# Optimization experiments

Measured on AMD Instinct MI355X. Metric: run time of the kernel, lower is better.

Reference implementation:

```python
import jax, jax.numpy as jnp
import numpy as np

B = 1024
P = 9            # patch_length
D = 2700         # d_model = input_dims = 30*30*3, num_heads=1 so d_k = D
DFF = 512
EPS = 1e-5


def setup_inputs() -> dict:
    key = jax.random.key(0)
    ks = jax.random.split(key, 32)
    s = 0.02
    inp = {
        "state": jax.random.normal(ks[0], (B, P * D), jnp.float32),
        "H1": jax.random.normal(ks[1], (B, P, DFF), jnp.float32),
        "H2": jax.random.normal(ks[2], (B, P, DFF), jnp.float32),
        # main projections: (in, out) layout for x @ W
        "Wq": jax.random.normal(ks[3], (D, D), jnp.float32) * s,
        "bq": jnp.zeros((D,), jnp.float32),
        "Wk": jax.random.normal(ks[4], (D, D), jnp.float32) * s,
        "bk": jnp.zeros((D,), jnp.float32),
        "Wv": jax.random.normal(ks[5], (D, D), jnp.float32) * s,
        "bv": jnp.zeros((D,), jnp.float32),
        # aux modulation projections from dff -> d_model
        "WC1q": jax.random.normal(ks[6], (DFF, D), jnp.float32) * s,
        "bC1q": jnp.zeros((D,), jnp.float32),
        "WC1k": jax.random.normal(ks[7], (DFF, D), jnp.float32) * s,
        "bC1k": jnp.zeros((D,), jnp.float32),
        "WC1v": jax.random.normal(ks[8], (DFF, D), jnp.float32) * s,
        "bC1v": jnp.zeros((D,), jnp.float32),
        "WC2q": jax.random.normal(ks[9], (DFF, D), jnp.float32) * s,
        "bC2q": jnp.zeros((D,), jnp.float32),
        "WC2k": jax.random.normal(ks[10], (DFF, D), jnp.float32) * s,
        "bC2k": jnp.zeros((D,), jnp.float32),
        "WC2v": jax.random.normal(ks[11], (DFF, D), jnp.float32) * s,
        "bC2v": jnp.zeros((D,), jnp.float32),
        # LayerNorm (norm1) affine params
        "gamma": jnp.ones((D,), jnp.float32),
        "beta": jnp.zeros((D,), jnp.float32),
    }
    return inp


def _layernorm(x, gamma, beta):
    mu = jnp.mean(x, axis=-1, keepdims=True)
    var = jnp.mean(jnp.square(x - mu), axis=-1, keepdims=True)
    return (x - mu) * jax.lax.rsqrt(var + EPS) * gamma + beta


def reference(state, H1, H2, Wq, bq, Wk, bk, Wv, bv,
              WC1q, bC1q, WC1k, bC1k, WC1v, bC1v,
              WC2q, bC2q, WC2k, bC2k, WC2v, bC2v,
              gamma, beta):
    x = state.reshape(-1, P, D)  # (B, 9, 2700)
    # elementwise-modulated Q/K/V (num_heads == 1)
    q = (x @ Wq + bq) * ((H1 @ WC1q + bC1q) + (H2 @ WC2q + bC2q))
    k = (x @ Wk + bk) * ((H1 @ WC1k + bC1k) + (H2 @ WC2k + bC2k))
    v = (x @ Wv + bv) * ((H1 @ WC1v + bC1v) + (H2 @ WC2v + bC2v))
    scale = 1.0 / jnp.sqrt(jnp.asarray(D, jnp.float32))
    scores = jnp.einsum("bqd,bkd->bqk", q, k) * scale  # (B, 9, 9)
    A = jax.nn.softmax(scores, axis=-1)
    attn = jnp.einsum("bqk,bkd->bqd", A, v)
    Z1 = x + attn  # dropout is identity in eval
    return _layernorm(Z1, gamma, beta)
```

## Files before the change

### kernel.cpp

```cpp
#include <hip/hip_runtime.h>
#include <stdint.h>


#define MROWS  9216
#define NCOLS  8192
#define KP1    2752
#define KP2    1024
#define DMODEL 2700

typedef __bf16 bf16x8 __attribute__((ext_vector_type(8)));
typedef float  f32x4  __attribute__((ext_vector_type(4)));

__device__ __forceinline__ float b2f(unsigned short u) {
  union { unsigned int u; float f; } v; v.u = ((unsigned int)u) << 16; return v.f;
}
__device__ __forceinline__ unsigned short f2b(float f) {
  union { float f; unsigned int u; } v; v.f = f;
  unsigned int r = v.u + 0x7FFFu + ((v.u >> 16) & 1u);
  return (unsigned short)(r >> 16);
}

__device__ __forceinline__ void gl2lds16(const void* g, void* l) {
  __builtin_amdgcn_global_load_lds(
      (const __attribute__((address_space(1))) void*)g,
      (__attribute__((address_space(3))) void*)l, 16, 0, 0);
}


__global__ void cvt_x(const float* __restrict__ src, unsigned short* __restrict__ dst) {
  int idx = blockIdx.x * 256 + threadIdx.x;
  int r = idx / KP1;
  int c = idx - r * KP1;
  float v = (c < DMODEL) ? src[(size_t)r * DMODEL + c] : 0.f;
  dst[idx] = f2b(v);
}

__global__ void cvt_h(const float* __restrict__ H1, const float* __restrict__ H2,
                      unsigned short* __restrict__ dst) {
  int idx = blockIdx.x * 256 + threadIdx.x;
  int r = idx >> 10, c = idx & 1023;
  float v = (c < 512) ? H1[r * 512 + c] : H2[r * 512 + (c - 512)];
  dst[idx] = f2b(v);
}

__global__ void cvt_wqkv(const float* __restrict__ Wq, const float* __restrict__ Wk,
                         const float* __restrict__ Wv, unsigned short* __restrict__ Wt) {
  __shared__ float tile[32][33];
  int k0 = blockIdx.x * 32, n0 = blockIdx.y * 32;
  int tx = threadIdx.x, ty = threadIdx.y;
#pragma unroll
  for (int s = 0; s < 4; s++) {
    int kk = k0 + ty + 8 * s, nn = n0 + tx;
    float v = 0.f;
    if (kk < DMODEL && nn < 3 * DMODEL) {
      int sec = (nn >= 5400) ? 2 : ((nn >= 2700) ? 1 : 0);
      int d = nn - sec * DMODEL;
      const float* W = (sec == 0) ? Wq : ((sec == 1) ? Wk : Wv);
      v = W[(size_t)kk * DMODEL + d];
    }
    tile[ty + 8 * s][tx] = v;
  }
  __syncthreads();
#pragma unroll
  for (int s = 0; s < 4; s++) {
    int nn = n0 + ty + 8 * s, kk = k0 + tx;
    Wt[(size_t)nn * KP1 + kk] = f2b(tile[tx][ty + 8 * s]);
  }
}

__global__ void cvt_wc(const float* __restrict__ C1q, const float* __restrict__ C1k,
                       const float* __restrict__ C1v, const float* __restrict__ C2q,
                       const float* __restrict__ C2k, const float* __restrict__ C2v,
                       unsigned short* __restrict__ Wt) {
  __shared__ float tile[32][33];
  int k0 = blockIdx.x * 32, n0 = blockIdx.y * 32;
  int tx = threadIdx.x, ty = threadIdx.y;
#pragma unroll
  for (int s = 0; s < 4; s++) {
    int kk = k0 + ty + 8 * s, nn = n0 + tx;
    float v = 0.f;
    if (nn < 3 * DMODEL) {
      int sec = (nn >= 5400) ? 2 : ((nn >= 2700) ? 1 : 0);
      int d = nn - sec * DMODEL;
      const float* W;
      int kr = kk;
      if (kk < 512) {
        W = (sec == 0) ? C1q : ((sec == 1) ? C1k : C1v);
      } else {
        W = (sec == 0) ? C2q : ((sec == 1) ? C2k : C2v);
        kr = kk - 512;
      }
      v = W[(size_t)kr * DMODEL + d];
    }
    tile[ty + 8 * s][tx] = v;
  }
  __syncthreads();
#pragma unroll
  for (int s = 0; s < 4; s++) {
    int nn = n0 + ty + 8 * s, kk = k0 + tx;
    Wt[(size_t)nn * KP2 + kk] = f2b(tile[tx][ty + 8 * s]);
  }
}

__global__ __launch_bounds__(256, 2) void gemm_fused(
    const unsigned short* __restrict__ Xb,
    const unsigned short* __restrict__ Wt,
    const unsigned short* __restrict__ Hb,
    const unsigned short* __restrict__ WCt,
    unsigned short* __restrict__ MQ,
    const float* __restrict__ bq_, const float* __restrict__ bk_, const float* __restrict__ bv_,
    const float* __restrict__ b1q, const float* __restrict__ b1k, const float* __restrict__ b1v,
    const float* __restrict__ b2q, const float* __restrict__ b2k, const float* __restrict__ b2v)
{
  __shared__ __align__(16) unsigned short As[128 * 64];
  __shared__ __align__(16) unsigned short Bs[128 * 64];
  const int tid = threadIdx.x;
  const int wave = tid >> 6, lane = tid & 63;
  const int m0 = blockIdx.y * 128, n0 = blockIdx.x * 128;
  const int wm = (wave >> 1) * 64, wn = (wave & 1) * 64;
  const int lm = lane & 15, lq = lane >> 4, l7 = lane & 7;

  int prow[4], pcl[4];
  unsigned int ldsoff[4];
#pragma unroll
  for (int r = 0; r < 4; r++) {
    int p = r * 256 + tid;
    prow[r] = p >> 3;
    pcl[r] = ((p & 7) ^ (prow[r] & 7)) * 8;
    ldsoff[r] = (unsigned int)p * 8;
  }

  f32x4 acc[4][4];
#pragma unroll
  for (int i = 0; i < 4; i++)
#pragma unroll
    for (int j = 0; j < 4; j++) acc[i][j] = (f32x4){0.f, 0.f, 0.f, 0.f};

  for (int k0 = 0; k0 < KP2; k0 += 64) {
#pragma unroll
    for (int r = 0; r < 4; r++) {
      gl2lds16(Hb + (size_t)(m0 + prow[r]) * KP2 + pcl[r] + k0, As + ldsoff[r]);
      gl2lds16(WCt + (size_t)(n0 + prow[r]) * KP2 + pcl[r] + k0, Bs + ldsoff[r]);
    }
    __syncthreads();
#pragma unroll
    for (int c = 0; c < 2; c++) {
      bf16x8 af[4], bfr[4];
      const int kx = (c * 4 + lq) ^ l7;
#pragma unroll
      for (int t = 0; t < 4; t++) {
        af[t]  = *(const bf16x8*)(As + (((wm + t * 16 + lm) << 3) + kx) * 8);
        bfr[t] = *(const bf16x8*)(Bs + (((wn + t * 16 + lm) << 3) + kx) * 8);
      }
#pragma unroll
      for (int mt = 0; mt < 4; mt++)
#pragma unroll
        for (int nt = 0; nt < 4; nt++)
          acc[mt][nt] = __builtin_amdgcn_mfma_f32_16x16x32_bf16(
              af[mt], bfr[nt], acc[mt][nt], 0, 0, 0);
    }
    __syncthreads();
  }

  unsigned int modp[4][4][2];
#pragma unroll
  for (int nt = 0; nt < 4; nt++) {
    int gc = n0 + wn + nt * 16 + lm;
    float bmod = 0.f;
    if (gc < 3 * DMODEL) {
      int sec = (gc >= 5400) ? 2 : ((gc >= 2700) ? 1 : 0);
      int d = gc - sec * DMODEL;
      const float* u1 = (sec == 0) ? b1q : ((sec == 1) ? b1k : b1v);
      const float* u2 = (sec == 0) ? b2q : ((sec == 1) ? b2k : b2v);
      bmod = u1[d] + u2[d];
    }
#pragma unroll
    for (int mt = 0; mt < 4; mt++) {
#pragma unroll
      for (int h = 0; h < 2; h++) {
        unsigned int lo = f2b(acc[mt][nt][2 * h] + bmod);
        unsigned int hi = f2b(acc[mt][nt][2 * h + 1] + bmod);
        modp[mt][nt][h] = lo | (hi << 16);
      }
    }
  }
#pragma unroll
  for (int i = 0; i < 4; i++)
#pragma unroll
    for (int j = 0; j < 4; j++) acc[i][j] = (f32x4){0.f, 0.f, 0.f, 0.f};

  for (int k0 = 0; k0 < KP1; k0 += 64) {
#pragma unroll
    for (int r = 0; r < 4; r++) {
      gl2lds16(Xb + (size_t)(m0 + prow[r]) * KP1 + pcl[r] + k0, As + ldsoff[r]);
      gl2lds16(Wt + (size_t)(n0 + prow[r]) * KP1 + pcl[r] + k0, Bs + ldsoff[r]);
    }
    __syncthreads();
#pragma unroll
    for (int c = 0; c < 2; c++) {
      bf16x8 af[4], bfr[4];
      const int kx = (c * 4 + lq) ^ l7;
#pragma unroll
      for (int t = 0; t < 4; t++) {
        af[t]  = *(const bf16x8*)(As + (((wm + t * 16 + lm) << 3) + kx) * 8);
        bfr[t] = *(const bf16x8*)(Bs + (((wn + t * 16 + lm) << 3) + kx) * 8);
      }
#pragma unroll
      for (int mt = 0; mt < 4; mt++)
#pragma unroll
        for (int nt = 0; nt < 4; nt++)
          acc[mt][nt] = __builtin_amdgcn_mfma_f32_16x16x32_bf16(
              af[mt], bfr[nt], acc[mt][nt], 0, 0, 0);
    }
    __syncthreads();
  }

#pragma unroll
  for (int nt = 0; nt < 4; nt++) {
    int gc = n0 + wn + nt * 16 + lm;
    float bmv = 0.f;
    if (gc < 3 * DMODEL) {
      int sec = (gc >= 5400) ? 2 : ((gc >= 2700) ? 1 : 0);
      int d = gc - sec * DMODEL;
      const float* bm = (sec == 0) ? bq_ : ((sec == 1) ? bk_ : bv_);
      bmv = bm[d];
    }
#pragma unroll
    for (int mt = 0; mt < 4; mt++) {
      int grb = m0 + wm + mt * 16 + lq * 4;
#pragma unroll
      for (int i = 0; i < 4; i++) {
        float mod = b2f((unsigned short)(modp[mt][nt][i >> 1] >> ((i & 1) * 16)));
        MQ[(size_t)(grb + i) * NCOLS + gc] = f2b((acc[mt][nt][i] + bmv) * mod);
      }
    }
  }
}

__global__ __launch_bounds__(256, 2) void attn_ln(
    const unsigned short* __restrict__ qkv,
    const float* __restrict__ x,
    const float* __restrict__ gamma, const float* __restrict__ beta,
    float* __restrict__ out)
{
  __shared__ float part[4][81];
  __shared__ float sc[81];
  __shared__ float redS[4][9], redQ[4][9];
  __shared__ float muL[9], rsL[9];

  const int b = blockIdx.x;
  const int tid = threadIdx.x, wave = tid >> 6, lane = tid & 63;
  const unsigned short* qb = qkv + (size_t)b * 9 * NCOLS;

  {
    const int l15 = lane & 15, lq8 = (lane >> 4) * 8;
    const int rA = (l15 < 9) ? l15 : 8;
    const unsigned short* qrow = qb + (size_t)rA * NCOLS;
    const unsigned short* krow = qb + (size_t)rA * NCOLS + DMODEL;
    f32x4 accS = (f32x4){0.f, 0.f, 0.f, 0.f};
    for (int s = wave; s < 85; s += 4) {
      int k0 = s * 32 + lq8;
      union { uint2 u[2]; unsigned int w[4]; bf16x8 v; } au, bu;
      au.u[0] = *(const uint2*)(qrow + k0);
      au.u[1] = *(const uint2*)(qrow + k0 + 4);
      bu.u[0] = *(const uint2*)(krow + k0);
      bu.u[1] = *(const uint2*)(krow + k0 + 4);
      if (s == 84) {
#pragma unroll
        for (int wd = 0; wd < 4; wd++)
          if (k0 + 2 * wd >= DMODEL) { au.w[wd] = 0u; bu.w[wd] = 0u; }
      }
      accS = __builtin_amdgcn_mfma_f32_16x16x32_bf16(au.v, bu.v, accS, 0, 0, 0);
    }
#pragma unroll
    for (int i = 0; i < 4; i++) {
      int row = (lane >> 4) * 4 + i, col = l15;
      if (row < 9 && col < 9) part[wave][row * 9 + col] = accS[i];
    }
  }
  __syncthreads();

  if (tid < 81)
    sc[tid] = (part[0][tid] + part[1][tid] + part[2][tid] + part[3][tid])
              * 0.019245008972987526f;
  __syncthreads();

  if (tid < 9) {
    float mx = -1e30f;
#pragma unroll
    for (int j = 0; j < 9; j++) mx = fmaxf(mx, sc[tid * 9 + j]);
    float e[9], sum = 0.f;
#pragma unroll
    for (int j = 0; j < 9; j++) { e[j] = __expf(sc[tid * 9 + j] - mx); sum += e[j]; }
    float inv = 1.f / sum;
#pragma unroll
    for (int j = 0; j < 9; j++) sc[tid * 9 + j] = e[j] * inv;
  }
  __syncthreads();

  float sum[9], sq[9];
#pragma unroll
  for (int i = 0; i < 9; i++) { sum[i] = 0.f; sq[i] = 0.f; }
  unsigned int pv[9][3][2];
#pragma unroll
  for (int c = 0; c < 3; c++) {
    int e = tid + c * 256;
    if (e < 675) {
      float4 t4[9];
#pragma unroll
      for (int i = 0; i < 9; i++)
        t4[i] = ((const float4*)(x + (size_t)(b * 9 + i) * DMODEL))[e];
#pragma unroll
      for (int j = 0; j < 9; j++) {
        ushort4 vv = ((const ushort4*)(qb + (size_t)j * NCOLS + 5400))[e];
        float v0 = b2f(vv.x), v1 = b2f(vv.y), v2 = b2f(vv.z), v3 = b2f(vv.w);
#pragma unroll
        for (int i = 0; i < 9; i++) {
          float p = sc[i * 9 + j];
          t4[i].x += p * v0; t4[i].y += p * v1;
          t4[i].z += p * v2; t4[i].w += p * v3;
        }
      }
#pragma unroll
      for (int i = 0; i < 9; i++) {
        sum[i] += t4[i].x + t4[i].y + t4[i].z + t4[i].w;
        sq[i]  += t4[i].x * t4[i].x + t4[i].y * t4[i].y
                + t4[i].z * t4[i].z + t4[i].w * t4[i].w;
        pv[i][c][0] = (unsigned int)f2b(t4[i].x) | ((unsigned int)f2b(t4[i].y) << 16);
        pv[i][c][1] = (unsigned int)f2b(t4[i].z) | ((unsigned int)f2b(t4[i].w) << 16);
      }
    }
  }

#pragma unroll
  for (int i = 0; i < 9; i++) {
    float s = sum[i], q = sq[i];
#pragma unroll
    for (int off = 32; off > 0; off >>= 1) {
      s += __shfl_down(s, off, 64);
      q += __shfl_down(q, off, 64);
    }
    if (lane == 0) { redS[wave][i] = s; redQ[wave][i] = q; }
  }
  __syncthreads();
  if (tid < 9) {
    float ts = redS[0][tid] + redS[1][tid] + redS[2][tid] + redS[3][tid];
    float tq = redQ[0][tid] + redQ[1][tid] + redQ[2][tid] + redQ[3][tid];
    float mu = ts * (1.f / 2700.f);
    muL[tid] = mu;
    rsL[tid] = rsqrtf(tq * (1.f / 2700.f) - mu * mu + 1e-5f);
  }
  __syncthreads();

#pragma unroll
  for (int c = 0; c < 3; c++) {
    int e = tid + c * 256;
    if (e < 675) {
      float4 g = ((const float4*)gamma)[e];
      float4 bb = ((const float4*)beta)[e];
#pragma unroll
      for (int i = 0; i < 9; i++) {
        float m = muL[i], r = rsL[i];
        float t0 = b2f((unsigned short)(pv[i][c][0] & 0xFFFF));
        float t1 = b2f((unsigned short)(pv[i][c][0] >> 16));
        float t2 = b2f((unsigned short)(pv[i][c][1] & 0xFFFF));
        float t3 = b2f((unsigned short)(pv[i][c][1] >> 16));
        float4 o;
        o.x = (t0 - m) * r * g.x + bb.x;
        o.y = (t1 - m) * r * g.y + bb.y;
        o.z = (t2 - m) * r * g.z + bb.z;
        o.w = (t3 - m) * r * g.w + bb.w;
        ((float4*)(out + (size_t)(b * 9 + i) * DMODEL))[e] = o;
      }
    }
  }
}

extern "C" void kernel_launch(void* const* d_in, const int* in_sizes, int n_in,
                              void* d_out, int out_size, void* d_ws, size_t ws_size,
                              hipStream_t stream) {
  const float* state = (const float*)d_in[0];
  const float* H1    = (const float*)d_in[1];
  const float* H2    = (const float*)d_in[2];
  const float* Wq    = (const float*)d_in[3];
  const float* bq    = (const float*)d_in[4];
  const float* Wk    = (const float*)d_in[5];
  const float* bk    = (const float*)d_in[6];
  const float* Wv    = (const float*)d_in[7];
  const float* bv    = (const float*)d_in[8];
  const float* WC1q  = (const float*)d_in[9];
  const float* bC1q  = (const float*)d_in[10];
  const float* WC1k  = (const float*)d_in[11];
  const float* bC1k  = (const float*)d_in[12];
  const float* WC1v  = (const float*)d_in[13];
  const float* bC1v  = (const float*)d_in[14];
  const float* WC2q  = (const float*)d_in[15];
  const float* bC2q  = (const float*)d_in[16];
  const float* WC2k  = (const float*)d_in[17];
  const float* bC2k  = (const float*)d_in[18];
  const float* WC2v  = (const float*)d_in[19];
  const float* bC2v  = (const float*)d_in[20];
  const float* gamma = (const float*)d_in[21];
  const float* beta  = (const float*)d_in[22];
  float* out = (float*)d_out;

  char* ws = (char*)d_ws;
  unsigned short* Xb  = (unsigned short*)(ws + 0);
  unsigned short* Wt  = (unsigned short*)(ws + 50724864);
  unsigned short* Hb  = (unsigned short*)(ws + 95813632);
  unsigned short* WCt = (unsigned short*)(ws + 114688000);
  unsigned short* MQ  = (unsigned short*)(ws + 131465216);

  cvt_x<<<dim3(MROWS * KP1 / 256), dim3(256), 0, stream>>>(state, Xb);
  cvt_wqkv<<<dim3(KP1 / 32, NCOLS / 32), dim3(32, 8), 0, stream>>>(Wq, Wk, Wv, Wt);
  cvt_h<<<dim3(MROWS * KP2 / 256), dim3(256), 0, stream>>>(H1, H2, Hb);
  cvt_wc<<<dim3(KP2 / 32, NCOLS / 32), dim3(32, 8), 0, stream>>>(WC1q, WC1k, WC1v,
                                                                 WC2q, WC2k, WC2v, WCt);

  gemm_fused<<<dim3(NCOLS / 128, MROWS / 128), dim3(256), 0, stream>>>(
      Xb, Wt, Hb, WCt, MQ, bq, bk, bv, bC1q, bC1k, bC1v, bC2q, bC2k, bC2v);

  attn_ln<<<dim3(1024), dim3(256), 0, stream>>>(MQ, state, gamma, beta, out);
}
```

Before: 1.107 ms.

## Vectorize conversion kernels, remap GEMM block order, widen attention-LN block

The x and H conversion kernels now convert 8 elements per thread, with float4 loads and 16-byte stores. The weight transpose kernels use 64x64 tiles with 256 threads and pack their bf16 output into 16-byte stores. The GEMM block index is remapped so each band of 8 N-tiles sweeps all 72 M-tiles, which should improve L2 reuse of the weight panels. The attention+LayerNorm kernel moves to 512 threads per block and keeps its intermediate values in LDS instead of registers, which raises parallelism per sample but uses about 48KB of LDS per block.

```diff
diff --git a/kernel.cpp b/kernel.cpp
--- a/kernel.cpp
+++ b/kernel.cpp
@@ -29,42 +29,77 @@
 
 __global__ void cvt_x(const float* __restrict__ src, unsigned short* __restrict__ dst) {
   int idx = blockIdx.x * 256 + threadIdx.x;
-  int r = idx / KP1;
-  int c = idx - r * KP1;
-  float v = (c < DMODEL) ? src[(size_t)r * DMODEL + c] : 0.f;
-  dst[idx] = f2b(v);
+  int r = idx / 344;
+  int c0 = (idx - r * 344) * 8;
+  uint4 o;
+  if (c0 + 8 <= DMODEL) {
+    const float4* p = (const float4*)(src + (size_t)r * DMODEL + c0);
+    float4 a = p[0], b = p[1];
+    o.x = f2b(a.x) | ((unsigned)f2b(a.y) << 16);
+    o.y = f2b(a.z) | ((unsigned)f2b(a.w) << 16);
+    o.z = f2b(b.x) | ((unsigned)f2b(b.y) << 16);
+    o.w = f2b(b.z) | ((unsigned)f2b(b.w) << 16);
+  } else {
+    unsigned short t[8];
+#pragma unroll
+    for (int j = 0; j < 8; j++) {
+      int c = c0 + j;
+      t[j] = (c < DMODEL) ? f2b(src[(size_t)r * DMODEL + c]) : (unsigned short)0;
+    }
+    o.x = t[0] | ((unsigned)t[1] << 16); o.y = t[2] | ((unsigned)t[3] << 16);
+    o.z = t[4] | ((unsigned)t[5] << 16); o.w = t[6] | ((unsigned)t[7] << 16);
+  }
+  *(uint4*)(dst + (size_t)r * KP1 + c0) = o;
 }
 
 __global__ void cvt_h(const float* __restrict__ H1, const float* __restrict__ H2,
                       unsigned short* __restrict__ dst) {
   int idx = blockIdx.x * 256 + threadIdx.x;
-  int r = idx >> 10, c = idx & 1023;
-  float v = (c < 512) ? H1[r * 512 + c] : H2[r * 512 + (c - 512)];
-  dst[idx] = f2b(v);
+  int r = idx >> 7;
+  int c0 = (idx & 127) * 8;
+  const float* srow = (c0 < 512) ? (H1 + (size_t)r * 512 + c0)
+                                 : (H2 + (size_t)r * 512 + (c0 - 512));
+  const float4* p = (const float4*)srow;
+  float4 a = p[0], b = p[1];
+  uint4 o;
+  o.x = f2b(a.x) | ((unsigned)f2b(a.y) << 16);
+  o.y = f2b(a.z) | ((unsigned)f2b(a.w) << 16);
+  o.z = f2b(b.x) | ((unsigned)f2b(b.y) << 16);
+  o.w = f2b(b.z) | ((unsigned)f2b(b.w) << 16);
+  *(uint4*)(dst + (size_t)r * KP2 + c0) = o;
 }
 
 __global__ void cvt_wqkv(const float* __restrict__ Wq, const float* __restrict__ Wk,
                          const float* __restrict__ Wv, unsigned short* __restrict__ Wt) {
-  __shared__ float tile[32][33];
-  int k0 = blockIdx.x * 32, n0 = blockIdx.y * 32;
-  int tx = threadIdx.x, ty = threadIdx.y;
-#pragma unroll
-  for (int s = 0; s < 4; s++) {
-    int kk = k0 + ty + 8 * s, nn = n0 + tx;
+  __shared__ float tile[64][65];
+  const int k0 = blockIdx.x * 64, n0 = blockIdx.y * 64;
+  const int tid = threadIdx.x;
+#pragma unroll
+  for (int i = 0; i < 16; i++) {
+    int e = tid + i * 256;
+    int kk = e >> 6, nn0 = e & 63;
+    int k = k0 + kk, nn = n0 + nn0;
     float v = 0.f;
-    if (kk < DMODEL && nn < 3 * DMODEL) {
+    if (k < DMODEL && nn < 3 * DMODEL) {
       int sec = (nn >= 5400) ? 2 : ((nn >= 2700) ? 1 : 0);
       int d = nn - sec * DMODEL;
       const float* W = (sec == 0) ? Wq : ((sec == 1) ? Wk : Wv);
-      v = W[(size_t)kk * DMODEL + d];
-    }
-    tile[ty + 8 * s][tx] = v;
-  }
-  __syncthreads();
-#pragma unroll
-  for (int s = 0; s < 4; s++) {
-    int nn = n0 + ty + 8 * s, kk = k0 + tx;
-    Wt[(size_t)nn * KP1 + kk] = f2b(tile[tx][ty + 8 * s]);
+      v = W[(size_t)k * DMODEL + d];
+    }
+    tile[kk][nn0] = v;
+  }
+  __syncthreads();
+  const int kc = (tid & 7) * 8;
+#pragma unroll
+  for (int i = 0; i < 2; i++) {
+    int nn0 = (tid >> 3) + i * 32;
+    uint4 o;
+    unsigned short t[8];
+#pragma unroll
+    for (int j = 0; j < 8; j++) t[j] = f2b(tile[kc + j][nn0]);
+    o.x = t[0] | ((unsigned)t[1] << 16); o.y = t[2] | ((unsigned)t[3] << 16);
+    o.z = t[4] | ((unsigned)t[5] << 16); o.w = t[6] | ((unsigned)t[7] << 16);
+    *(uint4*)(Wt + (size_t)(n0 + nn0) * KP1 + k0 + kc) = o;
   }
 }
 
@@ -72,33 +107,42 @@
                        const float* __restrict__ C1v, const float* __restrict__ C2q,
                        const float* __restrict__ C2k, const float* __restrict__ C2v,
                        unsigned short* __restrict__ Wt) {
-  __shared__ float tile[32][33];
-  int k0 = blockIdx.x * 32, n0 = blockIdx.y * 32;
-  int tx = threadIdx.x, ty = threadIdx.y;
-#pragma unroll
-  for (int s = 0; s < 4; s++) {
-    int kk = k0 + ty + 8 * s, nn = n0 + tx;
+  __shared__ float tile[64][65];
+  const int k0 = blockIdx.x * 64, n0 = blockIdx.y * 64;
+  const int tid = threadIdx.x;
+#pragma unroll
+  for (int i = 0; i < 16; i++) {
+    int e = tid + i * 256;
+    int kk = e >> 6, nn0 = e & 63;
+    int k = k0 + kk, nn = n0 + nn0;
     float v = 0.f;
     if (nn < 3 * DMODEL) {
       int sec = (nn >= 5400) ? 2 : ((nn >= 2700) ? 1 : 0);
       int d = nn - sec * DMODEL;
       const float* W;
-      int kr = kk;
-      if (kk < 512) {
+      int kr = k;
+      if (k < 512) {
         W = (sec == 0) ? C1q : ((sec == 1) ? C1k : C1v);
       } else {
         W = (sec == 0) ? C2q : ((sec == 1) ? C2k : C2v);
-        kr = kk - 512;
+        kr = k - 512;
       }
       v = W[(size_t)kr * DMODEL + d];
     }
-    tile[ty + 8 * s][tx] = v;
-  }
-  __syncthreads();
-#pragma unroll
-  for (int s = 0; s < 4; s++) {
-    int nn = n0 + ty + 8 * s, kk = k0 + tx;
-    Wt[(size_t)nn * KP2 + kk] = f2b(tile[tx][ty + 8 * s]);
+    tile[kk][nn0] = v;
+  }
+  __syncthreads();
+  const int kc = (tid & 7) * 8;
+#pragma unroll
+  for (int i = 0; i < 2; i++) {
+    int nn0 = (tid >> 3) + i * 32;
+    uint4 o;
+    unsigned short t[8];
+#pragma unroll
+    for (int j = 0; j < 8; j++) t[j] = f2b(tile[kc + j][nn0]);
+    o.x = t[0] | ((unsigned)t[1] << 16); o.y = t[2] | ((unsigned)t[3] << 16);
+    o.z = t[4] | ((unsigned)t[5] << 16); o.w = t[6] | ((unsigned)t[7] << 16);
+    *(uint4*)(Wt + (size_t)(n0 + nn0) * KP2 + k0 + kc) = o;
   }
 }
 
@@ -116,7 +160,14 @@
   __shared__ __align__(16) unsigned short Bs[128 * 64];
   const int tid = threadIdx.x;
   const int wave = tid >> 6, lane = tid & 63;
-  const int m0 = blockIdx.y * 128, n0 = blockIdx.x * 128;
+
+  const int id = blockIdx.y * 64 + blockIdx.x;
+  const int band = id / 576;
+  const int rem = id - band * 576;
+  const int mt_ = rem % 72;
+  const int ntl = rem / 72;
+  const int m0 = mt_ * 128, n0 = (band * 8 + ntl) * 128;
+
   const int wm = (wave >> 1) * 64, wn = (wave & 1) * 64;
   const int lm = lane & 15, lq = lane >> 4, l7 = lane & 7;
 
@@ -237,15 +288,16 @@
   }
 }
 
-__global__ __launch_bounds__(256, 2) void attn_ln(
+__global__ __launch_bounds__(512, 4) void attn_ln(
     const unsigned short* __restrict__ qkv,
     const float* __restrict__ x,
     const float* __restrict__ gamma, const float* __restrict__ beta,
     float* __restrict__ out)
 {
-  __shared__ float part[4][81];
+  __shared__ unsigned int tlds[9 * 675 * 2];
+  __shared__ float part[8][81];
   __shared__ float sc[81];
-  __shared__ float redS[4][9], redQ[4][9];
+  __shared__ float redS[8][9], redQ[8][9];
   __shared__ float muL[9], rsL[9];
 
   const int b = blockIdx.x;
@@ -258,7 +310,7 @@
     const unsigned short* qrow = qb + (size_t)rA * NCOLS;
     const unsigned short* krow = qb + (size_t)rA * NCOLS + DMODEL;
     f32x4 accS = (f32x4){0.f, 0.f, 0.f, 0.f};
-    for (int s = wave; s < 85; s += 4) {
+    for (int s = wave; s < 85; s += 8) {
       int k0 = s * 32 + lq8;
       union { uint2 u[2]; unsigned int w[4]; bf16x8 v; } au, bu;
       au.u[0] = *(const uint2*)(qrow + k0);
@@ -280,9 +332,12 @@
   }
   __syncthreads();
 
-  if (tid < 81)
-    sc[tid] = (part[0][tid] + part[1][tid] + part[2][tid] + part[3][tid])
-              * 0.019245008972987526f;
+  if (tid < 81) {
+    float s = 0.f;
+#pragma unroll
+    for (int w = 0; w < 8; w++) s += part[w][tid];
+    sc[tid] = s * 0.019245008972987526f;
+  }
   __syncthreads();
 
   if (tid < 9) {
@@ -301,10 +356,9 @@
   float sum[9], sq[9];
 #pragma unroll
   for (int i = 0; i < 9; i++) { sum[i] = 0.f; sq[i] = 0.f; }
-  unsigned int pv[9][3][2];
-#pragma unroll
-  for (int c = 0; c < 3; c++) {
-    int e = tid + c * 256;
+#pragma unroll
+  for (int c = 0; c < 2; c++) {
+    int e = tid + c * 512;
     if (e < 675) {
       float4 t4[9];
 #pragma unroll
@@ -326,8 +380,10 @@
         sum[i] += t4[i].x + t4[i].y + t4[i].z + t4[i].w;
         sq[i]  += t4[i].x * t4[i].x + t4[i].y * t4[i].y
                 + t4[i].z * t4[i].z + t4[i].w * t4[i].w;
-        pv[i][c][0] = (unsigned int)f2b(t4[i].x) | ((unsigned int)f2b(t4[i].y) << 16);
-        pv[i][c][1] = (unsigned int)f2b(t4[i].z) | ((unsigned int)f2b(t4[i].w) << 16);
+        uint2 pk;
+        pk.x = (unsigned int)f2b(t4[i].x) | ((unsigned int)f2b(t4[i].y) << 16);
+        pk.y = (unsigned int)f2b(t4[i].z) | ((unsigned int)f2b(t4[i].w) << 16);
+        *(uint2*)&tlds[(i * 675 + e) * 2] = pk;
       }
     }
   }
@@ -344,8 +400,9 @@
   }
   __syncthreads();
   if (tid < 9) {
-    float ts = redS[0][tid] + redS[1][tid] + redS[2][tid] + redS[3][tid];
-    float tq = redQ[0][tid] + redQ[1][tid] + redQ[2][tid] + redQ[3][tid];
+    float ts = 0.f, tq = 0.f;
+#pragma unroll
+    for (int w = 0; w < 8; w++) { ts += redS[w][tid]; tq += redQ[w][tid]; }
     float mu = ts * (1.f / 2700.f);
     muL[tid] = mu;
     rsL[tid] = rsqrtf(tq * (1.f / 2700.f) - mu * mu + 1e-5f);
@@ -353,18 +410,19 @@
   __syncthreads();
 
 #pragma unroll
-  for (int c = 0; c < 3; c++) {
-    int e = tid + c * 256;
+  for (int c = 0; c < 2; c++) {
+    int e = tid + c * 512;
     if (e < 675) {
       float4 g = ((const float4*)gamma)[e];
       float4 bb = ((const float4*)beta)[e];
 #pragma unroll
       for (int i = 0; i < 9; i++) {
         float m = muL[i], r = rsL[i];
-        float t0 = b2f((unsigned short)(pv[i][c][0] & 0xFFFF));
-        float t1 = b2f((unsigned short)(pv[i][c][0] >> 16));
-        float t2 = b2f((unsigned short)(pv[i][c][1] & 0xFFFF));
-        float t3 = b2f((unsigned short)(pv[i][c][1] >> 16));
+        uint2 pk = *(const uint2*)&tlds[(i * 675 + e) * 2];
+        float t0 = b2f((unsigned short)(pk.x & 0xFFFF));
+        float t1 = b2f((unsigned short)(pk.x >> 16));
+        float t2 = b2f((unsigned short)(pk.y & 0xFFFF));
+        float t3 = b2f((unsigned short)(pk.y >> 16));
         float4 o;
         o.x = (t0 - m) * r * g.x + bb.x;
         o.y = (t1 - m) * r * g.y + bb.y;
@@ -411,14 +469,14 @@
   unsigned short* WCt = (unsigned short*)(ws + 114688000);
   unsigned short* MQ  = (unsigned short*)(ws + 131465216);
 
-  cvt_x<<<dim3(MROWS * KP1 / 256), dim3(256), 0, stream>>>(state, Xb);
-  cvt_wqkv<<<dim3(KP1 / 32, NCOLS / 32), dim3(32, 8), 0, stream>>>(Wq, Wk, Wv, Wt);
-  cvt_h<<<dim3(MROWS * KP2 / 256), dim3(256), 0, stream>>>(H1, H2, Hb);
-  cvt_wc<<<dim3(KP2 / 32, NCOLS / 32), dim3(32, 8), 0, stream>>>(WC1q, WC1k, WC1v,
-                                                                 WC2q, WC2k, WC2v, WCt);
-
-  gemm_fused<<<dim3(NCOLS / 128, MROWS / 128), dim3(256), 0, stream>>>(
+  cvt_x<<<dim3(9216 * 344 / 256), dim3(256), 0, stream>>>(state, Xb);
+  cvt_wqkv<<<dim3(43, 128), dim3(256), 0, stream>>>(Wq, Wk, Wv, Wt);
+  cvt_h<<<dim3(9216 * 128 / 256), dim3(256), 0, stream>>>(H1, H2, Hb);
+  cvt_wc<<<dim3(16, 128), dim3(256), 0, stream>>>(WC1q, WC1k, WC1v,
+                                                  WC2q, WC2k, WC2v, WCt);
+
+  gemm_fused<<<dim3(64, 72), dim3(256), 0, stream>>>(
       Xb, Wt, Hb, WCt, MQ, bq, bk, bv, bC1q, bC1k, bC1v, bC2q, bC2k, bC2v);
 
-  attn_ln<<<dim3(1024), dim3(256), 0, stream>>>(MQ, state, gamma, beta, out);
-}
+  attn_ln<<<dim3(1024), dim3(512), 0, stream>>>(MQ, state, gamma, beta, out);
+}
```

Result: no change. 1.116 ms (+0.8%).
